# Kernel tuning notes

Measured on AMD Instinct MI355X. Metric: run time of the kernel, lower is better.

## Reference

```python
import jax, jax.numpy as jnp
import numpy as np

BATCH = 512
SEQ = 500          # number of time points; SEQ-1 spline pieces
INPUT_CH = 8       # input (control) channels
HIDDEN = 64        # hidden channels (size of z)
HH = 128           # hidden_hidden channels of the CDE func MLP
OUT = 1            # output channels


def setup_inputs() -> dict:
    key = jax.random.key(0)
    ks = jax.random.split(key, 12)
    shp = (BATCH, SEQ - 1, INPUT_CH)
    times = jnp.linspace(0.0, 1.0, SEQ, dtype=jnp.float32)
    coeff_a = jax.random.normal(ks[0], shp, dtype=jnp.float32)
    coeff_b = jax.random.normal(ks[1], shp, dtype=jnp.float32)
    coeff_two_c = jax.random.normal(ks[2], shp, dtype=jnp.float32)
    coeff_three_d = jax.random.normal(ks[3], shp, dtype=jnp.float32)
    # learned parameters
    init_W = jax.random.normal(ks[4], (INPUT_CH, HIDDEN), dtype=jnp.float32) / np.sqrt(INPUT_CH)
    init_b = jnp.zeros((HIDDEN,), dtype=jnp.float32)
    f_W1 = jax.random.normal(ks[5], (HIDDEN, HH), dtype=jnp.float32) / np.sqrt(HIDDEN)
    f_b1 = jnp.zeros((HH,), dtype=jnp.float32)
    f_W2 = jax.random.normal(ks[6], (HH, HIDDEN * INPUT_CH), dtype=jnp.float32) / np.sqrt(HH)
    f_b2 = jnp.zeros((HIDDEN * INPUT_CH,), dtype=jnp.float32)
    lin_W = jax.random.normal(ks[7], (HIDDEN, OUT), dtype=jnp.float32) / np.sqrt(HIDDEN)
    lin_b = jnp.zeros((OUT,), dtype=jnp.float32)
    return dict(times=times, coeff_a=coeff_a, coeff_b=coeff_b,
                coeff_two_c=coeff_two_c, coeff_three_d=coeff_three_d,
                init_W=init_W, init_b=init_b, f_W1=f_W1, f_b1=f_b1,
                f_W2=f_W2, f_b2=f_b2, lin_W=lin_W, lin_b=lin_b)


def reference(times, coeff_a, coeff_b, coeff_two_c, coeff_three_d,
              init_W, init_b, f_W1, f_b1, f_W2, f_b2, lin_W, lin_b):
    n_pieces = coeff_b.shape[1]

    def _interpret_t(t):
        idx = jnp.clip(jnp.sum(t > times) - 1, 0, n_pieces - 1)
        frac = t - times[idx]
        return frac, idx

    def spline_eval(t):  # NaturalCubicSpline.evaluate -> (B, INPUT_CH)
        frac, idx = _interpret_t(t)
        inner = 0.5 * coeff_two_c[:, idx] + coeff_three_d[:, idx] * frac / 3.0
        inner = coeff_b[:, idx] + inner * frac
        return coeff_a[:, idx] + inner * frac

    def dX_dt(t):  # NaturalCubicSpline.derivative -> (B, INPUT_CH)
        frac, idx = _interpret_t(t)
        inner = coeff_two_c[:, idx] + coeff_three_d[:, idx] * frac
        return coeff_b[:, idx] + inner * frac

    def f(z):  # CDE vector field MLP -> (B, HIDDEN, INPUT_CH)
        h = jax.nn.relu(z @ f_W1 + f_b1)
        v = jnp.tanh(h @ f_W2 + f_b2)
        return v.reshape(z.shape[0], HIDDEN, INPUT_CH)

    def F(t, z):  # VectorField: f(z) @ dX/dt -> (B, HIDDEN)
        return jnp.einsum('bhi,bi->bh', f(z), dX_dt(t))

    # initial state from initial_network applied to X(t0)
    z0 = spline_eval(times[0]) @ init_W + init_b  # (B, HIDDEN)

    @jax.checkpoint
    def rk4_step(z, i):
        t0 = times[i]
        h = times[i + 1] - times[i]
        k1 = F(t0, z)
        k2 = F(t0 + 0.5 * h, z + 0.5 * h * k1)
        k3 = F(t0 + 0.5 * h, z + 0.5 * h * k2)
        k4 = F(t0 + h, z + h * k3)
        z_next = z + (h / 6.0) * (k1 + 2.0 * k2 + 2.0 * k3 + k4)
        return z_next, None

    zT, _ = jax.lax.scan(rk4_step, z0, jnp.arange(SEQ - 1))
    # final linear readout + sigmoid activation
    return jax.nn.sigmoid(zT @ lin_W + lin_b)  # (B, OUT)
```

## Files before the change

kernel.cpp:

```cpp
#include <hip/hip_runtime.h>

#define NPIECE 499
#define SEQN 500

typedef __attribute__((ext_vector_type(8))) short bf16x8;
typedef __attribute__((ext_vector_type(4))) short s16x4;
typedef __attribute__((ext_vector_type(4))) float f32x4;

__device__ inline short f2bf(float x) {
    union { float f; unsigned u; } v; v.f = x;
    unsigned r = v.u + 0x7FFFu + ((v.u >> 16) & 1u);
    return (short)(r >> 16);
}

__device__ inline float fast_tanh(float x) {
    float e = __expf(2.0f * x);
    return 1.0f - 2.0f * __builtin_amdgcn_rcpf(e + 1.0f);
}

__global__ void __launch_bounds__(512, 2)
cde_kernel(const float* __restrict__ times,
           const float* __restrict__ ca,  const float* __restrict__ cb,
           const float* __restrict__ c2c, const float* __restrict__ c3d,
           const float* __restrict__ initW, const float* __restrict__ initb,
           const float* __restrict__ W1,  const float* __restrict__ b1,
           const float* __restrict__ W2,  const float* __restrict__ b2,
           const float* __restrict__ linW, const float* __restrict__ linb,
           float* __restrict__ out)
{
    const int tid  = threadIdx.x;
    const int lane = tid & 63;
    const int wv   = tid >> 6;
    const int g    = lane >> 4;
    const int col  = lane & 15;
    const int g0   = g & 1, g1 = g >> 1;
    const int s0   = blockIdx.x * 16;

    __shared__ __align__(16) float tl[SEQN];
    __shared__ __align__(16) short zflat[8][16][8];
    __shared__ __align__(16) short hflat[16][16][8];
    __shared__ __align__(16) float dxl[2][3][2][16][4];
    __shared__ __align__(16) float zinit[64][16];
    __shared__ __align__(16) float pred[8][16];

    for (int j = tid; j < SEQN; j += 512) tl[j] = times[j];

    bf16x8 a2[4][4];
    float  b2f[4][4];
#pragma unroll
    for (int tt = 0; tt < 4; ++tt) {
        const int o = 16 * (4 * wv + tt) + col;
#pragma unroll
        for (int kk = 0; kk < 4; ++kk) {
            bf16x8 f;
#pragma unroll
            for (int e = 0; e < 8; ++e)
                f[e] = f2bf(W2[(32 * kk + 8 * g + e) * 512 + o]);
            a2[tt][kk] = f;
        }
#pragma unroll
        for (int r = 0; r < 4; ++r)
            b2f[tt][r] = b2[16 * (4 * wv + tt) + 4 * g + r];
    }
    bf16x8 a1[2];
    float  b1f[4];
    {
        const int o = 16 * wv + col;
#pragma unroll
        for (int kk = 0; kk < 2; ++kk) {
            bf16x8 f;
#pragma unroll
            for (int e = 0; e < 8; ++e)
                f[e] = f2bf(W1[(32 * kk + 8 * g + e) * 128 + o]);
            a1[kk] = f;
        }
#pragma unroll
        for (int r = 0; r < 4; ++r) b1f[r] = b1[16 * wv + 4 * g + r];
    }

    __syncthreads();

#pragma unroll
    for (int v = 0; v < 2; ++v) {
        const int idx = tid * 2 + v, hid = idx >> 4, sm = idx & 15;
        float z = initb[hid];
#pragma unroll
        for (int c = 0; c < 8; ++c)
            z += ca[((size_t)(s0 + sm)) * (NPIECE * 8) + c] * initW[c * 64 + hid];
        zinit[hid][sm] = z;
        zflat[hid >> 3][sm][hid & 7] = f2bf(z);
    }
    const int pslot = tid >> 7, prr = tid & 127, psm = prr >> 3, pch = prr & 7;
    const size_t prow = ((size_t)(s0 + psm)) * (NPIECE * 8);
    if (tid < 384) {
        float t0n = tl[0], t1n = tl[1], hn = t1n - t0n; int p; float fr;
        if (pslot == 0)      { p = 0; fr = 0.0f; }
        else if (pslot == 1) { p = 0; fr = (t0n + 0.5f * hn) - t0n; }
        else { float t3 = t0n + hn;
               if (t3 > t1n) { p = 1; fr = t3 - t1n; } else { p = 0; fr = t3 - t0n; } }
        const size_t off = prow + (size_t)p * 8 + pch;
        dxl[0][pslot][pch >> 2][psm][pch & 3] = cb[off] + (c2c[off] + c3d[off] * fr) * fr;
    }
    __syncthreads();

    const bool owner = ((lane & 31) < 16);
    const int hi = lane >> 5;
    float zreg[4], zs[4];
#pragma unroll
    for (int tt = 0; tt < 4; ++tt) {
        zs[tt] = 0.f;
        zreg[tt] = zinit[8 * wv + 2 * tt + hi][col];
    }

    for (int i = 0; i < NPIECE; ++i) {
        const float hs = tl[i + 1] - tl[i];
        const int par = i & 1;

        float pb = 0.f, pc = 0.f, pd = 0.f, pfr = 0.f;
        const bool pf = (i + 1 < NPIECE) && (tid < 384);
        if (pf) {
            const int j = i + 1;
            float t0n = tl[j], t1n = tl[j + 1], hn = t1n - t0n; int p; float fr;
            if (pslot == 0)      { p = j - 1; fr = t0n - tl[j - 1]; }
            else if (pslot == 1) { p = j; fr = (t0n + 0.5f * hn) - t0n; }
            else { float t3 = t0n + hn;
                   if (j < NPIECE - 1 && t3 > t1n) { p = j + 1; fr = t3 - t1n; }
                   else                            { p = j;     fr = t3 - t0n; } }
            const size_t off = prow + (size_t)p * 8 + pch;
            pb = cb[off]; pc = c2c[off]; pd = c3d[off]; pfr = fr;
        }

#pragma unroll
        for (int st = 0; st < 4; ++st) {
            const int dsel = (st == 0) ? 0 : ((st == 3) ? 2 : 1);
            __syncthreads();

            if (st == 3 && pf)
                dxl[par ^ 1][pslot][pch >> 2][psm][pch & 3] = pb + (pc + pd * pfr) * pfr;

            bf16x8 bz0 = *(const bf16x8*)&zflat[g][col][0];
            bf16x8 bz1 = *(const bf16x8*)&zflat[4 + g][col][0];
            f32x4 ha = {b1f[0], b1f[1], b1f[2], b1f[3]};
            ha = __builtin_amdgcn_mfma_f32_16x16x32_bf16(a1[0], bz0, ha, 0, 0, 0);
            ha = __builtin_amdgcn_mfma_f32_16x16x32_bf16(a1[1], bz1, ha, 0, 0, 0);
            s16x4 wout;
#pragma unroll
            for (int r = 0; r < 4; ++r) wout[r] = f2bf(fmaxf(ha[r], 0.f));
            *(s16x4*)&hflat[2 * wv + g1][col][4 * g0] = wout;
            __syncthreads();

            bf16x8 bh[4];
#pragma unroll
            for (int c = 0; c < 4; ++c)
                bh[c] = *(const bf16x8*)&hflat[4 * c + g][col][0];
            f32x4 cc[4];
#pragma unroll
            for (int tt = 0; tt < 4; ++tt) cc[tt] = (f32x4){0.f, 0.f, 0.f, 0.f};
#pragma unroll
            for (int kk = 0; kk < 4; ++kk)
#pragma unroll
                for (int tt = 0; tt < 4; ++tt)
                    cc[tt] = __builtin_amdgcn_mfma_f32_16x16x32_bf16(a2[tt][kk], bh[kk], cc[tt], 0, 0, 0);

            f32x4 dd = *(const f32x4*)&dxl[par][dsel][g0][col][0];
            float pt[4];
#pragma unroll
            for (int tt = 0; tt < 4; ++tt) {
                float s = 0.f;
#pragma unroll
                for (int r = 0; r < 4; ++r)
                    s += fast_tanh(cc[tt][r] + b2f[tt][r]) * dd[r];
                pt[tt] = s;
            }
#pragma unroll
            for (int tt = 0; tt < 4; ++tt)
                pt[tt] += __shfl_xor(pt[tt], 16);

            if (owner) {
#pragma unroll
                for (int tt = 0; tt < 4; ++tt) {
                    const float k = pt[tt];
                    float zst;
                    if (st == 0)      { zs[tt] = k;          zst = zreg[tt] + 0.5f * hs * k; }
                    else if (st == 1) { zs[tt] += 2.f * k;   zst = zreg[tt] + 0.5f * hs * k; }
                    else if (st == 2) { zs[tt] += 2.f * k;   zst = zreg[tt] + hs * k; }
                    else              { zs[tt] += k;         zst = zreg[tt] + (hs / 6.f) * zs[tt];
                                        zreg[tt] = zst; }
                    zflat[wv][col][2 * tt + hi] = f2bf(zst);
                }
            }
        }
    }

    float p = 0.f;
#pragma unroll
    for (int tt = 0; tt < 4; ++tt) p += zreg[tt] * linW[8 * wv + 2 * tt + hi];
    p += __shfl_xor(p, 32);
    if (lane < 16) pred[wv][col] = p;
    __syncthreads();
    if (tid < 16) {
        float a = linb[0];
#pragma unroll
        for (int w = 0; w < 8; ++w) a += pred[w][tid];
        out[s0 + tid] = 1.0f / (1.0f + __expf(-a));
    }
}

extern "C" void kernel_launch(void* const* d_in, const int* in_sizes, int n_in,
                              void* d_out, int out_size, void* d_ws, size_t ws_size,
                              hipStream_t stream) {
    (void)in_sizes; (void)n_in; (void)d_ws; (void)ws_size; (void)out_size;
    const float* times = (const float*)d_in[0];
    const float* ca    = (const float*)d_in[1];
    const float* cb    = (const float*)d_in[2];
    const float* c2c   = (const float*)d_in[3];
    const float* c3d   = (const float*)d_in[4];
    const float* initW = (const float*)d_in[5];
    const float* initb = (const float*)d_in[6];
    const float* W1    = (const float*)d_in[7];
    const float* b1    = (const float*)d_in[8];
    const float* W2    = (const float*)d_in[9];
    const float* b2    = (const float*)d_in[10];
    const float* linW  = (const float*)d_in[11];
    const float* linb  = (const float*)d_in[12];
    cde_kernel<<<32, 512, 0, stream>>>(times, ca, cb, c2c, c3d, initW, initb,
                                       W1, b1, W2, b2, linW, linb, (float*)d_out);
}
```

Measured before the change: 2.181 ms.

## Compute full hidden layer per wave to remove a barrier per RK stage

```diff
diff --git a/kernel.cpp b/kernel.cpp
--- a/kernel.cpp
+++ b/kernel.cpp
@@ -4,13 +4,18 @@
 #define SEQN 500
 
 typedef __attribute__((ext_vector_type(8))) short bf16x8;
-typedef __attribute__((ext_vector_type(4))) short s16x4;
 typedef __attribute__((ext_vector_type(4))) float f32x4;
 
 __device__ inline short f2bf(float x) {
     union { float f; unsigned u; } v; v.f = x;
     unsigned r = v.u + 0x7FFFu + ((v.u >> 16) & 1u);
     return (short)(r >> 16);
+}
+
+__device__ inline unsigned cvt_pk(float lo, float hi) {
+    unsigned r;
+    asm("v_cvt_pk_bf16_f32 %0, %1, %2" : "=v"(r) : "v"(lo), "v"(hi));
+    return r;
 }
 
 __device__ inline float fast_tanh(float x) {
@@ -33,12 +38,12 @@
     const int wv   = tid >> 6;
     const int g    = lane >> 4;
     const int col  = lane & 15;
-    const int g0   = g & 1, g1 = g >> 1;
+    const int g0   = g & 1;
+    const int hi   = lane >> 5;
     const int s0   = blockIdx.x * 16;
 
     __shared__ __align__(16) float tl[SEQN];
-    __shared__ __align__(16) short zflat[8][16][8];
-    __shared__ __align__(16) short hflat[16][16][8];
+    __shared__ __align__(16) short zflat[2][8][16][8];
     __shared__ __align__(16) float dxl[2][3][2][16][4];
     __shared__ __align__(16) float zinit[64][16];
     __shared__ __align__(16) float pred[8][16];
@@ -46,36 +51,40 @@
     for (int j = tid; j < SEQN; j += 512) tl[j] = times[j];
 
     bf16x8 a2[4][4];
-    float  b2f[4][4];
+    f32x4  b2f[4];
 #pragma unroll
     for (int tt = 0; tt < 4; ++tt) {
         const int o = 16 * (4 * wv + tt) + col;
 #pragma unroll
-        for (int kk = 0; kk < 4; ++kk) {
+        for (int c = 0; c < 4; ++c) {
             bf16x8 f;
 #pragma unroll
-            for (int e = 0; e < 8; ++e)
-                f[e] = f2bf(W2[(32 * kk + 8 * g + e) * 512 + o]);
-            a2[tt][kk] = f;
+            for (int e = 0; e < 8; ++e) {
+                const int q = 32 * c + 16 * (e >> 2) + 4 * g + (e & 3);
+                f[e] = f2bf(W2[q * 512 + o]);
+            }
+            a2[tt][c] = f;
         }
 #pragma unroll
         for (int r = 0; r < 4; ++r)
             b2f[tt][r] = b2[16 * (4 * wv + tt) + 4 * g + r];
     }
-    bf16x8 a1[2];
-    float  b1f[4];
-    {
-        const int o = 16 * wv + col;
-#pragma unroll
-        for (int kk = 0; kk < 2; ++kk) {
+    bf16x8 a1[8][2];
+    f32x4  b1f[8];
+#pragma unroll
+    for (int t = 0; t < 8; ++t) {
+#pragma unroll
+        for (int c = 0; c < 2; ++c) {
             bf16x8 f;
 #pragma unroll
-            for (int e = 0; e < 8; ++e)
-                f[e] = f2bf(W1[(32 * kk + 8 * g + e) * 128 + o]);
-            a1[kk] = f;
-        }
-#pragma unroll
-        for (int r = 0; r < 4; ++r) b1f[r] = b1[16 * wv + 4 * g + r];
+            for (int e = 0; e < 8; ++e) {
+                const int p = 32 * c + 8 * g + 2 * (e & 3) + (e >> 2);
+                f[e] = f2bf(W1[p * 128 + 16 * t + col]);
+            }
+            a1[t][c] = f;
+        }
+#pragma unroll
+        for (int r = 0; r < 4; ++r) b1f[t][r] = b1[16 * t + 4 * g + r];
     }
 
     __syncthreads();
@@ -88,7 +97,7 @@
         for (int c = 0; c < 8; ++c)
             z += ca[((size_t)(s0 + sm)) * (NPIECE * 8) + c] * initW[c * 64 + hid];
         zinit[hid][sm] = z;
-        zflat[hid >> 3][sm][hid & 7] = f2bf(z);
+        zflat[0][hid >> 3][sm][4 * (hid & 1) + ((hid & 7) >> 1)] = f2bf(z);
     }
     const int pslot = tid >> 7, prr = tid & 127, psm = prr >> 3, pch = prr & 7;
     const size_t prow = ((size_t)(s0 + psm)) * (NPIECE * 8);
@@ -103,8 +112,6 @@
     }
     __syncthreads();
 
-    const bool owner = ((lane & 31) < 16);
-    const int hi = lane >> 5;
     float zreg[4], zs[4];
 #pragma unroll
     for (int tt = 0; tt < 4; ++tt) {
@@ -130,64 +137,79 @@
             pb = cb[off]; pc = c2c[off]; pd = c3d[off]; pfr = fr;
         }
 
+        f32x4 ddr0, ddr1, ddr2;
 #pragma unroll
         for (int st = 0; st < 4; ++st) {
-            const int dsel = (st == 0) ? 0 : ((st == 3) ? 2 : 1);
+            const int rb = st & 1, wb = rb ^ 1;
             __syncthreads();
 
+            if (st == 0) {
+                ddr0 = *(const f32x4*)&dxl[par][0][g0][col][0];
+                ddr1 = *(const f32x4*)&dxl[par][1][g0][col][0];
+                ddr2 = *(const f32x4*)&dxl[par][2][g0][col][0];
+            }
             if (st == 3 && pf)
                 dxl[par ^ 1][pslot][pch >> 2][psm][pch & 3] = pb + (pc + pd * pfr) * pfr;
 
-            bf16x8 bz0 = *(const bf16x8*)&zflat[g][col][0];
-            bf16x8 bz1 = *(const bf16x8*)&zflat[4 + g][col][0];
-            f32x4 ha = {b1f[0], b1f[1], b1f[2], b1f[3]};
-            ha = __builtin_amdgcn_mfma_f32_16x16x32_bf16(a1[0], bz0, ha, 0, 0, 0);
-            ha = __builtin_amdgcn_mfma_f32_16x16x32_bf16(a1[1], bz1, ha, 0, 0, 0);
-            s16x4 wout;
-#pragma unroll
-            for (int r = 0; r < 4; ++r) wout[r] = f2bf(fmaxf(ha[r], 0.f));
-            *(s16x4*)&hflat[2 * wv + g1][col][4 * g0] = wout;
-            __syncthreads();
-
-            bf16x8 bh[4];
+            bf16x8 bz0 = *(const bf16x8*)&zflat[rb][g][col][0];
+            bf16x8 bz1 = *(const bf16x8*)&zflat[rb][4 + g][col][0];
+            f32x4 ha[8];
+#pragma unroll
+            for (int t = 0; t < 8; ++t)
+                ha[t] = __builtin_amdgcn_mfma_f32_16x16x32_bf16(a1[t][0], bz0, b1f[t], 0, 0, 0);
+#pragma unroll
+            for (int t = 0; t < 8; ++t)
+                ha[t] = __builtin_amdgcn_mfma_f32_16x16x32_bf16(a1[t][1], bz1, ha[t], 0, 0, 0);
+
+            union { bf16x8 v; unsigned u[4]; } bh[4];
+#pragma unroll
+            for (int c = 0; c < 4; ++c) {
+                bh[c].u[0] = cvt_pk(fmaxf(ha[2 * c][0], 0.f), fmaxf(ha[2 * c][1], 0.f));
+                bh[c].u[1] = cvt_pk(fmaxf(ha[2 * c][2], 0.f), fmaxf(ha[2 * c][3], 0.f));
+                bh[c].u[2] = cvt_pk(fmaxf(ha[2 * c + 1][0], 0.f), fmaxf(ha[2 * c + 1][1], 0.f));
+                bh[c].u[3] = cvt_pk(fmaxf(ha[2 * c + 1][2], 0.f), fmaxf(ha[2 * c + 1][3], 0.f));
+            }
+
+            f32x4 cc[4];
+#pragma unroll
+            for (int tt = 0; tt < 4; ++tt) cc[tt] = (f32x4){0.f, 0.f, 0.f, 0.f};
 #pragma unroll
             for (int c = 0; c < 4; ++c)
-                bh[c] = *(const bf16x8*)&hflat[4 * c + g][col][0];
-            f32x4 cc[4];
-#pragma unroll
-            for (int tt = 0; tt < 4; ++tt) cc[tt] = (f32x4){0.f, 0.f, 0.f, 0.f};
-#pragma unroll
-            for (int kk = 0; kk < 4; ++kk)
 #pragma unroll
                 for (int tt = 0; tt < 4; ++tt)
-                    cc[tt] = __builtin_amdgcn_mfma_f32_16x16x32_bf16(a2[tt][kk], bh[kk], cc[tt], 0, 0, 0);
-
-            f32x4 dd = *(const f32x4*)&dxl[par][dsel][g0][col][0];
+                    cc[tt] = __builtin_amdgcn_mfma_f32_16x16x32_bf16(a2[tt][c], bh[c].v, cc[tt], 0, 0, 0);
+
+            f32x4 dd = (st == 0) ? ddr0 : ((st == 3) ? ddr2 : ddr1);
             float pt[4];
 #pragma unroll
             for (int tt = 0; tt < 4; ++tt) {
-                float s = 0.f;
+                float sacc = 0.f;
 #pragma unroll
                 for (int r = 0; r < 4; ++r)
-                    s += fast_tanh(cc[tt][r] + b2f[tt][r]) * dd[r];
-                pt[tt] = s;
+                    sacc += fast_tanh(cc[tt][r] + b2f[tt][r]) * dd[r];
+                pt[tt] = sacc;
             }
 #pragma unroll
             for (int tt = 0; tt < 4; ++tt)
                 pt[tt] += __shfl_xor(pt[tt], 16);
 
-            if (owner) {
-#pragma unroll
-                for (int tt = 0; tt < 4; ++tt) {
-                    const float k = pt[tt];
-                    float zst;
-                    if (st == 0)      { zs[tt] = k;          zst = zreg[tt] + 0.5f * hs * k; }
-                    else if (st == 1) { zs[tt] += 2.f * k;   zst = zreg[tt] + 0.5f * hs * k; }
-                    else if (st == 2) { zs[tt] += 2.f * k;   zst = zreg[tt] + hs * k; }
-                    else              { zs[tt] += k;         zst = zreg[tt] + (hs / 6.f) * zs[tt];
-                                        zreg[tt] = zst; }
-                    zflat[wv][col][2 * tt + hi] = f2bf(zst);
-                }
+            float zw[4];
+#pragma unroll
+            for (int tt = 0; tt < 4; ++tt) {
+                const float k = pt[tt];
+                float zst;
+                if (st == 0)      { zs[tt] = k;          zst = zreg[tt] + 0.5f * hs * k; }
+                else if (st == 1) { zs[tt] += 2.f * k;   zst = zreg[tt] + 0.5f * hs * k; }
+                else if (st == 2) { zs[tt] += 2.f * k;   zst = zreg[tt] + hs * k; }
+                else              { zs[tt] += k;         zst = zreg[tt] + (hs / 6.f) * zs[tt];
+                                    zreg[tt] = zst; }
+                zw[tt] = zst;
+            }
+            if (!(lane & 16)) {
+                int2 wdat;
+                wdat.x = (int)cvt_pk(zw[0], zw[1]);
+                wdat.y = (int)cvt_pk(zw[2], zw[3]);
+                *(int2*)&zflat[wb][wv][col][4 * hi] = wdat;
             }
         }
     }
```

Result: slower. 2.608 ms (+19.6%).
